# Performance work log

Measured on AMD Instinct MI355X. Metric: run time of the kernel, lower is better.

The kernel has to match this reference:

```python
import jax, jax.numpy as jnp
import numpy as np


def _phi(x):
    # ELU(x) + 1 feature map (positive kernel feature map)
    return jax.nn.elu(x) + 1.0


def setup_inputs() -> dict:
    key = jax.random.key(0)
    k1, k2, k3 = jax.random.split(key, 3)
    B, S, E = 4, 4096, 1024
    inputs = jax.random.normal(k1, (B, S, E), dtype=jnp.float32)
    mask = jnp.ones((B, S), dtype=jnp.float32)
    w_qkv = jax.random.normal(k2, (3 * E, E), dtype=jnp.float32) * (E ** -0.5)
    b_qkv = jax.random.normal(k3, (3 * E,), dtype=jnp.float32) * 0.02
    return {"inputs": inputs, "mask": mask, "w_qkv": w_qkv, "b_qkv": b_qkv, "num_heads": 16}


def reference(inputs, mask, w_qkv, b_qkv, num_heads):
    B, S, E = inputs.shape
    H = num_heads
    D = E // H
    # qkv projection: torch Linear is x @ W.T + b
    qkv = inputs @ w_qkv.T + b_qkv                     # (B, S, 3E)
    qkv = qkv.reshape(B, S, 3, H, D)
    q = qkv[:, :, 0]                                   # (B, S, H, D)
    k = qkv[:, :, 1]
    v = qkv[:, :, 2]
    # key masking (float multiply, as in einsum 'bshd,bs->bshd')
    k = k * mask[:, :, None, None]
    kq = _phi(q)                                       # (B, S, H, D)
    kk = _phi(k)                                       # (B, S, H, D)
    # kv outer-product accumulation over sequence: (B, H, M, D)
    kv = jnp.einsum('bshd,bshm->bhmd', kk, v)
    # normalizer
    z = 1.0 / (jnp.einsum('bshd,bhd->bsh', kq, kk.sum(axis=1)) + 1e-6)
    # final contraction
    attn = jnp.einsum('bshd,bhmd,bsh->bshm', kq, kv, z)  # (B, S, H, D)
    attn = attn.reshape(B, S, E)
    # NOTE: original forward computes a projection but returns `attn` (dropout is
    # identity at inference), so projection is dead code and omitted here.
    return attn
```

## Files before the change

### kernel.cpp

```cpp
#include <hip/hip_runtime.h>

typedef unsigned short u16;
typedef short bf16x8 __attribute__((ext_vector_type(8)));
typedef float f32x4 __attribute__((ext_vector_type(4)));
typedef u16 u16x8 __attribute__((ext_vector_type(8)));
typedef u16 u16x4 __attribute__((ext_vector_type(4)));

#define B_ 4
#define S_ 4096
#define E_ 1024
#define H_ 16
#define D_ 64
#define M_ 16384
#define N_ 3072
#define K_ 1024

__device__ __forceinline__ u16 f2b(float f) {
    unsigned x = __builtin_bit_cast(unsigned, f);
    return (u16)((x + 0x7fffu + ((x >> 16) & 1u)) >> 16);
}
__device__ __forceinline__ float b2f(u16 u) {
    unsigned x = ((unsigned)u) << 16;
    return __builtin_bit_cast(float, x);
}
__device__ __forceinline__ float phi_f(float x) { return x > 0.f ? x + 1.f : __expf(x); }

__device__ __forceinline__ void gload16(const void* g, void* l) {
    __builtin_amdgcn_global_load_lds((const __attribute__((address_space(1))) void*)g,
                                     (__attribute__((address_space(3))) void*)l, 16, 0, 0);
}

__global__ void cvt_bf16(const float* __restrict__ in, u16* __restrict__ out, int n8) {
    int stride = gridDim.x * blockDim.x;
    for (int i = blockIdx.x * blockDim.x + threadIdx.x; i < n8; i += stride) {
        const float4* p = (const float4*)(in + (size_t)i * 8);
        float4 a = p[0], b = p[1];
        u16x8 o;
        o[0] = f2b(a.x); o[1] = f2b(a.y); o[2] = f2b(a.z); o[3] = f2b(a.w);
        o[4] = f2b(b.x); o[5] = f2b(b.y); o[6] = f2b(b.z); o[7] = f2b(b.w);
        *(u16x8*)(out + (size_t)i * 8) = o;
    }
}


__device__ __forceinline__ void compute_tile(const char* ldsbase, int rowA, int rowB,
                                             int pc0, int pc1, f32x4 (&acc)[8][4])
{
    const char* bA = ldsbase + rowA;
    const char* bB = ldsbase + 32768 + rowB;
#pragma unroll
    for (int kk = 0; kk < 2; ++kk) {
        int pc = kk ? pc1 : pc0;
        bf16x8 a[8], bb[4];
#pragma unroll
        for (int mi = 0; mi < 8; ++mi) a[mi] = *(const bf16x8*)(bA + mi * 2048 + pc);
#pragma unroll
        for (int ni = 0; ni < 4; ++ni) bb[ni] = *(const bf16x8*)(bB + ni * 2048 + pc);
        __builtin_amdgcn_s_setprio(1);
#pragma unroll
        for (int mi = 0; mi < 8; ++mi)
#pragma unroll
            for (int ni = 0; ni < 4; ++ni)
                acc[mi][ni] = __builtin_amdgcn_mfma_f32_16x16x32_bf16(
                    a[mi], bb[ni], acc[mi][ni], 0, 0, 0);
        __builtin_amdgcn_s_setprio(0);
    }
}

__device__ __forceinline__ void stage_tile(const u16* gA, const u16* gB, char* ldsbase, int t)
{
#pragma unroll
    for (int i = 0; i < 4; ++i)
        gload16(gA + (size_t)i * 64 * K_, ldsbase + i * 8192 + t * 16);
#pragma unroll
    for (int i = 0; i < 4; ++i)
        gload16(gB + (size_t)i * 64 * K_, ldsbase + 32768 + i * 8192 + t * 16);
}

#define MEMFENCE asm volatile("" ::: "memory")

__global__ __launch_bounds__(512, 2) void gemm_qkv(
    const u16* __restrict__ Abf, const u16* __restrict__ Wbf,
    const float* __restrict__ bias, const float* __restrict__ mask,
    u16* __restrict__ KQ, u16* __restrict__ KKT, u16* __restrict__ VT)
{
    __shared__ __align__(16) char lds[131072];

    int wg  = blockIdx.x;
    int xcd = wg & 7, ii = wg >> 3;
    int tm  = xcd * 8 + ii / 12;
    int tn  = ii % 12;
    int m0 = tm << 8, n0 = tn << 8;

    int t = threadIdx.x;
    int l = t & 63, wid = t >> 6;
    int wr = wid >> 2, wc = wid & 3;
    int lg = l >> 4, lr = l & 15;

    int srow  = t >> 3;
    int scolE = ((t & 7) ^ (srow & 7)) << 3;
    const u16* gA = Abf + (size_t)(m0 + srow) * K_ + scolE;
    const u16* gB = Wbf + (size_t)(n0 + srow) * K_ + scolE;

    int rowA = (wr * 128 + lr) * 128;
    int rowB = (wc * 64 + lr) * 128;
    int pc0  = (lg * 16) ^ ((lr & 7) << 4);
    int pc1  = pc0 ^ 64;

    f32x4 acc[8][4] = {};

    stage_tile(gA, gB, lds, t);
    stage_tile(gA + 64, gB + 64, lds + 65536, t);
    asm volatile("s_waitcnt vmcnt(8)" ::: "memory");
    __builtin_amdgcn_s_barrier();
    MEMFENCE;

    for (int kt2 = 0; kt2 < 14; kt2 += 2) {
        compute_tile(lds, rowA, rowB, pc0, pc1, acc);
        MEMFENCE;
        __builtin_amdgcn_s_barrier();
        MEMFENCE;
        stage_tile(gA + (size_t)(kt2 + 2) * 64, gB + (size_t)(kt2 + 2) * 64, lds, t);
        asm volatile("s_waitcnt vmcnt(8)" ::: "memory");
        __builtin_amdgcn_s_barrier();
        MEMFENCE;
        compute_tile(lds + 65536, rowA, rowB, pc0, pc1, acc);
        MEMFENCE;
        __builtin_amdgcn_s_barrier();
        MEMFENCE;
        stage_tile(gA + (size_t)(kt2 + 3) * 64, gB + (size_t)(kt2 + 3) * 64, lds + 65536, t);
        asm volatile("s_waitcnt vmcnt(8)" ::: "memory");
        __builtin_amdgcn_s_barrier();
        MEMFENCE;
    }
    compute_tile(lds, rowA, rowB, pc0, pc1, acc);
    asm volatile("s_waitcnt vmcnt(0)" ::: "memory");
    __builtin_amdgcn_s_barrier();
    MEMFENCE;
    compute_tile(lds + 65536, rowA, rowB, pc0, pc1, acc);

    int part = n0 >> 10;

    float bv[4];
#pragma unroll
    for (int ni = 0; ni < 4; ++ni) bv[ni] = bias[n0 + wc * 64 + ni * 16 + lr];

    if (part == 0) {
#pragma unroll
        for (int mi = 0; mi < 8; ++mi)
#pragma unroll
            for (int j = 0; j < 4; ++j) {
                int row = m0 + wr * 128 + mi * 16 + lg * 4 + j;
#pragma unroll
                for (int ni = 0; ni < 4; ++ni) {
                    int col = n0 + wc * 64 + ni * 16 + lr;
                    KQ[(size_t)row * E_ + col] = f2b(phi_f(acc[mi][ni][j] + bv[ni]));
                }
            }
    } else {
        u16* dst0 = (part == 1) ? KKT : VT;
        int b  = m0 >> 12;
        int sl = m0 & (S_ - 1);
        int h  = ((tn & 3) << 2) | wc;
#pragma unroll
        for (int mi = 0; mi < 8; ++mi) {
            int sbase = sl + wr * 128 + mi * 16 + lg * 4;
            float mk[4];
#pragma unroll
            for (int j = 0; j < 4; ++j)
                mk[j] = (part == 1) ? mask[m0 + wr * 128 + mi * 16 + lg * 4 + j] : 1.f;
#pragma unroll
            for (int ni = 0; ni < 4; ++ni) {
                u16x4 o;
#pragma unroll
                for (int j = 0; j < 4; ++j) {
                    float v = acc[mi][ni][j] + bv[ni];
                    if (part == 1) v = phi_f(v * mk[j]);
                    o[j] = f2b(v);
                }
                int d = ni * 16 + lr;
                *(u16x4*)(dst0 + ((size_t)((b * H_ + h) * D_ + d)) * S_ + sbase) = o;
            }
        }
    }
}

__global__ __launch_bounds__(256) void kv_ksum_partial(
    const u16* __restrict__ VT, const u16* __restrict__ KKT,
    float* __restrict__ KVP, float* __restrict__ KSP)
{
    __shared__ __align__(16) u16 smem[8192];
    u16* As = smem;
    u16* Bs = smem + 4096;
    int bh = blockIdx.x;
    int ch = blockIdx.y;
    int s0 = ch << 8;
    int t = threadIdx.x;
    int l = t & 63, w = t >> 6;
    int lg = l >> 4, lr = l & 15;
    const u16* Ag = VT + (size_t)bh * (D_ * S_);
    const u16* Bg = KKT + (size_t)bh * (D_ * S_);
    int srow = t >> 3, scol = (t & 7) << 3;

    f32x4 acc[4] = {};
    float ks = 0.f;
    int kd = t >> 2;
    int kq4 = (t & 3) << 4;

    for (int kt = 0; kt < 4; ++kt) {
        __syncthreads();
        int sb = s0 + kt * 64;
#pragma unroll
        for (int i = 0; i < 2; ++i) {
            gload16(Ag + (size_t)(srow + i * 32) * S_ + sb + scol, As + i * 2048 + t * 8);
            gload16(Bg + (size_t)(srow + i * 32) * S_ + sb + scol, Bs + i * 2048 + t * 8);
        }
        __syncthreads();
#pragma unroll
        for (int i = 0; i < 16; ++i) ks += b2f(Bs[kd * 64 + kq4 + i]);
#pragma unroll
        for (int kh = 0; kh < 2; ++kh) {
            int ko = kh * 32 + lg * 8;
            bf16x8 a = *(const bf16x8*)&As[(w * 16 + lr) * 64 + ko];
#pragma unroll
            for (int ni = 0; ni < 4; ++ni) {
                bf16x8 bb = *(const bf16x8*)&Bs[(ni * 16 + lr) * 64 + ko];
                acc[ni] = __builtin_amdgcn_mfma_f32_16x16x32_bf16(a, bb, acc[ni], 0, 0, 0);
            }
        }
    }
    float* kvp = KVP + (size_t)ch * (64 * 4096) + bh * 4096;
#pragma unroll
    for (int ni = 0; ni < 4; ++ni)
#pragma unroll
        for (int j = 0; j < 4; ++j)
            kvp[(w * 16 + lg * 4 + j) * 64 + ni * 16 + lr] = acc[ni][j];
    ks += __shfl_xor(ks, 1);
    ks += __shfl_xor(ks, 2);
    if ((t & 3) == 0) KSP[ch * 4096 + bh * 64 + kd] = ks;
}

__global__ void reduce_kv(const float* __restrict__ KVP, const float* __restrict__ KSP,
                          float* __restrict__ KV, float* __restrict__ KSUM)
{
    int g = blockIdx.x * 256 + threadIdx.x;
#pragma unroll 1
    for (int i = g * 4; i < g * 4 + 4; ++i) {
        float s = 0.f;
#pragma unroll
        for (int c = 0; c < 16; ++c) s += KVP[(size_t)c * (64 * 4096) + i];
        KV[i] = s;
    }
    if (g < 4096) {
        float s = 0.f;
#pragma unroll
        for (int c = 0; c < 16; ++c) s += KSP[c * 4096 + g];
        KSUM[g] = s;
    }
}

__global__ __launch_bounds__(256) void attn_out(
    const u16* __restrict__ KQ, const float* __restrict__ KV,
    const float* __restrict__ KSUM, float* __restrict__ Out)
{
    __shared__ __align__(16) u16 kqs[16384];
    __shared__ __align__(16) u16 bsm[5120];
    __shared__ float den[256];
    int bh = blockIdx.x, ch = blockIdx.y;
    int b = bh >> 4, h = bh & 15;
    int t = threadIdx.x;
    int l = t & 63, w = t >> 6;
    int lg = l >> 4, lr = l & 15;
    size_t row0 = (size_t)b * S_ + ch * 256;
    int srow = t >> 3, scol = (t & 7) << 3;
#pragma unroll
    for (int i = 0; i < 8; ++i)
        gload16(KQ + (row0 + srow + i * 32) * E_ + h * 64 + scol, kqs + i * 2048 + t * 8);

    const float* kvg = KV + bh * 4096;
#pragma unroll
    for (int ii = 0; ii < 16; ii += 4) {
        float4 v = *(const float4*)(kvg + t * 16 + ii);
        u16x4 o; o[0] = f2b(v.x); o[1] = f2b(v.y); o[2] = f2b(v.z); o[3] = f2b(v.w);
        *(u16x4*)&bsm[t * 16 + ii] = o;
    }
    if (t < 64) bsm[4096 + t] = f2b(KSUM[bh * 64 + t]);
    for (int i = t; i < 960; i += 256) bsm[4160 + i] = 0;
    __syncthreads();

    f32x4 acc[4][5] = {};
#pragma unroll
    for (int kh = 0; kh < 2; ++kh) {
        int ko = kh * 32 + lg * 8;
        bf16x8 af[4];
#pragma unroll
        for (int mi = 0; mi < 4; ++mi)
            af[mi] = *(const bf16x8*)&kqs[(w * 64 + mi * 16 + lr) * 64 + ko];
#pragma unroll
        for (int ni = 0; ni < 5; ++ni) {
            bf16x8 bb = *(const bf16x8*)&bsm[(ni * 16 + lr) * 64 + ko];
#pragma unroll
            for (int mi = 0; mi < 4; ++mi)
                acc[mi][ni] = __builtin_amdgcn_mfma_f32_16x16x32_bf16(af[mi], bb, acc[mi][ni], 0, 0, 0);
        }
    }
    if (lr == 0) {
#pragma unroll
        for (int mi = 0; mi < 4; ++mi)
#pragma unroll
            for (int j = 0; j < 4; ++j)
                den[w * 64 + mi * 16 + lg * 4 + j] = acc[mi][4][j];
    }
    __syncthreads();
#pragma unroll
    for (int mi = 0; mi < 4; ++mi)
#pragma unroll
        for (int j = 0; j < 4; ++j) {
            int sl = w * 64 + mi * 16 + lg * 4 + j;
            float z = 1.f / (den[sl] + 1e-6f);
            float* op = Out + (row0 + sl) * E_ + h * 64;
#pragma unroll
            for (int ni = 0; ni < 4; ++ni)
                op[ni * 16 + lr] = acc[mi][ni][j] * z;
        }
}

extern "C" void kernel_launch(void* const* d_in, const int* in_sizes, int n_in,
                              void* d_out, int out_size, void* d_ws, size_t ws_size,
                              hipStream_t stream)
{
    const float* inputs = (const float*)d_in[0];
    const float* mask   = (const float*)d_in[1];
    const float* w_qkv  = (const float*)d_in[2];
    const float* b_qkv  = (const float*)d_in[3];

    u16* Abf = (u16*)d_ws;
    u16* Wbf = Abf + (size_t)M_ * K_;
    u16* KQ  = Wbf + (size_t)N_ * K_;
    float* KVP  = (float*)(KQ + (size_t)M_ * E_);
    float* KSP  = KVP + 16 * 64 * 4096;
    float* KV   = KSP + 16 * 4096;
    float* KSUM = KV + 64 * 4096;

    u16* KKT = (u16*)d_out;
    u16* VT  = KKT + (size_t)M_ * E_;

    cvt_bf16<<<2048, 256, 0, stream>>>(inputs, Abf, M_ * K_ / 8);
    cvt_bf16<<<768, 256, 0, stream>>>(w_qkv, Wbf, N_ * K_ / 8);
    gemm_qkv<<<768, 512, 0, stream>>>(Abf, Wbf, b_qkv, mask, KQ, KKT, VT);
    kv_ksum_partial<<<dim3(64, 16), 256, 0, stream>>>(VT, KKT, KVP, KSP);
    reduce_kv<<<256, 256, 0, stream>>>(KVP, KSP, KV, KSUM);
    attn_out<<<dim3(64, 16), 256, 0, stream>>>(KQ, KV, KSUM, (float*)d_out);
}
```

Before: 168.6 us.

## Interleave LDS reads, global-to-LDS staging and MFMA in fine-grained GEMM sub-stages

Restructures the QKV GEMM main loop into eight sub-stages per double-buffered tile pair. Each sub-stage reads a quarter of the A/B fragments from LDS, issues part of the next tile's global-to-LDS loads, and runs a 4x2 MFMA block, with barriers between them. A and B staging are split so B can be prefetched into the other buffer earlier. The aim is to overlap memory traffic with matrix math in a ping-pong schedule. In exchange it adds many more barriers and redundant clamped tail loads (tiles 15) that must stay correct with the vmcnt accounting.

```diff
diff --git a/kernel.cpp b/kernel.cpp
--- a/kernel.cpp
+++ b/kernel.cpp
@@ -29,6 +29,8 @@
     __builtin_amdgcn_global_load_lds((const __attribute__((address_space(1))) void*)g,
                                      (__attribute__((address_space(3))) void*)l, 16, 0, 0);
 }
+
+#define MEMFENCE asm volatile("" ::: "memory")
 
 __global__ void cvt_bf16(const float* __restrict__ in, u16* __restrict__ out, int n8) {
     int stride = gridDim.x * blockDim.x;
@@ -43,42 +45,6 @@
 }
 
 
-__device__ __forceinline__ void compute_tile(const char* ldsbase, int rowA, int rowB,
-                                             int pc0, int pc1, f32x4 (&acc)[8][4])
-{
-    const char* bA = ldsbase + rowA;
-    const char* bB = ldsbase + 32768 + rowB;
-#pragma unroll
-    for (int kk = 0; kk < 2; ++kk) {
-        int pc = kk ? pc1 : pc0;
-        bf16x8 a[8], bb[4];
-#pragma unroll
-        for (int mi = 0; mi < 8; ++mi) a[mi] = *(const bf16x8*)(bA + mi * 2048 + pc);
-#pragma unroll
-        for (int ni = 0; ni < 4; ++ni) bb[ni] = *(const bf16x8*)(bB + ni * 2048 + pc);
-        __builtin_amdgcn_s_setprio(1);
-#pragma unroll
-        for (int mi = 0; mi < 8; ++mi)
-#pragma unroll
-            for (int ni = 0; ni < 4; ++ni)
-                acc[mi][ni] = __builtin_amdgcn_mfma_f32_16x16x32_bf16(
-                    a[mi], bb[ni], acc[mi][ni], 0, 0, 0);
-        __builtin_amdgcn_s_setprio(0);
-    }
-}
-
-__device__ __forceinline__ void stage_tile(const u16* gA, const u16* gB, char* ldsbase, int t)
-{
-#pragma unroll
-    for (int i = 0; i < 4; ++i)
-        gload16(gA + (size_t)i * 64 * K_, ldsbase + i * 8192 + t * 16);
-#pragma unroll
-    for (int i = 0; i < 4; ++i)
-        gload16(gB + (size_t)i * 64 * K_, ldsbase + 32768 + i * 8192 + t * 16);
-}
-
-#define MEMFENCE asm volatile("" ::: "memory")
-
 __global__ __launch_bounds__(512, 2) void gemm_qkv(
     const u16* __restrict__ Abf, const u16* __restrict__ Wbf,
     const float* __restrict__ bias, const float* __restrict__ mask,
@@ -99,45 +65,68 @@
 
     int srow  = t >> 3;
     int scolE = ((t & 7) ^ (srow & 7)) << 3;
+    int t16   = t * 16;
+
     const u16* gA = Abf + (size_t)(m0 + srow) * K_ + scolE;
     const u16* gB = Wbf + (size_t)(n0 + srow) * K_ + scolE;
 
-    int rowA = (wr * 128 + lr) * 128;
-    int rowB = (wc * 64 + lr) * 128;
-    int pc0  = (lg * 16) ^ ((lr & 7) << 4);
-    int pc1  = pc0 ^ 64;
+    const char* aB = lds + (wr * 128 + lr) * 128;
+    const char* bB = lds + 32768 + (wc * 64 + lr) * 128;
+    int pc0 = (lg * 16) ^ ((lr & 7) << 4);
+    int pc1 = pc0 ^ 64;
 
     f32x4 acc[8][4] = {};
-
-    stage_tile(gA, gB, lds, t);
-    stage_tile(gA + 64, gB + 64, lds + 65536, t);
-    asm volatile("s_waitcnt vmcnt(8)" ::: "memory");
+    bf16x8 av[4][2], bv2[2][2];
+
+#define RD_A(BO, MI0) { _Pragma("unroll") for (int m_ = 0; m_ < 4; ++m_) { \
+    av[m_][0] = *(const bf16x8*)(aB + (BO) + (MI0 + m_) * 2048 + pc0); \
+    av[m_][1] = *(const bf16x8*)(aB + (BO) + (MI0 + m_) * 2048 + pc1); } }
+
+#define RD_B(BO, NI0) { _Pragma("unroll") for (int n_ = 0; n_ < 2; ++n_) { \
+    bv2[n_][0] = *(const bf16x8*)(bB + (BO) + (NI0 + n_) * 2048 + pc0); \
+    bv2[n_][1] = *(const bf16x8*)(bB + (BO) + (NI0 + n_) * 2048 + pc1); } }
+
+#define ST_A(TT, HI, BO) { \
+    gload16(gA + (size_t)((HI) * 64) * K_ + (TT) * 64, lds + (BO) + (HI) * 8192 + t16); \
+    gload16(gA + (size_t)((HI) * 64 + 128) * K_ + (TT) * 64, lds + (BO) + 16384 + (HI) * 8192 + t16); }
+
+#define ST_B(TT, PR, BO) { \
+    gload16(gB + (size_t)((PR) * 128) * K_ + (TT) * 64, lds + (BO) + 32768 + (PR) * 16384 + t16); \
+    gload16(gB + (size_t)((PR) * 128 + 64) * K_ + (TT) * 64, lds + (BO) + 32768 + (PR) * 16384 + 8192 + t16); }
+
+#define BAR { MEMFENCE; __builtin_amdgcn_s_barrier(); MEMFENCE; }
+
+#define MM(MI0, NI0) { __builtin_amdgcn_s_setprio(1); \
+    _Pragma("unroll") for (int m_ = 0; m_ < 4; ++m_) \
+    _Pragma("unroll") for (int n_ = 0; n_ < 2; ++n_) \
+    _Pragma("unroll") for (int h_ = 0; h_ < 2; ++h_) \
+        acc[(MI0) + m_][(NI0) + n_] = __builtin_amdgcn_mfma_f32_16x16x32_bf16( \
+            av[m_][h_], bv2[n_][h_], acc[(MI0) + m_][(NI0) + n_], 0, 0, 0); \
+    __builtin_amdgcn_s_setprio(0); }
+
+    ST_A(0, 0, 0); ST_A(0, 1, 0); ST_B(0, 0, 0); ST_B(0, 1, 0);
+    ST_A(1, 0, 65536); ST_A(1, 1, 65536);
+    asm volatile("s_waitcnt vmcnt(4)" ::: "memory");
     __builtin_amdgcn_s_barrier();
     MEMFENCE;
 
-    for (int kt2 = 0; kt2 < 14; kt2 += 2) {
-        compute_tile(lds, rowA, rowB, pc0, pc1, acc);
-        MEMFENCE;
-        __builtin_amdgcn_s_barrier();
-        MEMFENCE;
-        stage_tile(gA + (size_t)(kt2 + 2) * 64, gB + (size_t)(kt2 + 2) * 64, lds, t);
-        asm volatile("s_waitcnt vmcnt(8)" ::: "memory");
-        __builtin_amdgcn_s_barrier();
-        MEMFENCE;
-        compute_tile(lds + 65536, rowA, rowB, pc0, pc1, acc);
-        MEMFENCE;
-        __builtin_amdgcn_s_barrier();
-        MEMFENCE;
-        stage_tile(gA + (size_t)(kt2 + 3) * 64, gB + (size_t)(kt2 + 3) * 64, lds + 65536, t);
-        asm volatile("s_waitcnt vmcnt(8)" ::: "memory");
-        __builtin_amdgcn_s_barrier();
-        MEMFENCE;
-    }
-    compute_tile(lds, rowA, rowB, pc0, pc1, acc);
-    asm volatile("s_waitcnt vmcnt(0)" ::: "memory");
-    __builtin_amdgcn_s_barrier();
-    MEMFENCE;
-    compute_tile(lds + 65536, rowA, rowB, pc0, pc1, acc);
+#pragma unroll 1
+    for (int kt = 0; kt < 16; kt += 2) {
+        int tp2 = kt + 2 < 16 ? kt + 2 : 15;
+        int tp3 = kt + 3 < 16 ? kt + 3 : 15;
+        RD_A(0, 0); RD_B(0, 0); ST_B(kt + 1, 0, 65536); BAR; MM(0, 0); BAR;
+        RD_B(0, 2); ST_B(kt + 1, 1, 65536); BAR; MM(0, 2); BAR;
+        RD_A(0, 4); ST_A(tp2, 0, 0); BAR; MM(4, 2); BAR;
+        RD_B(0, 0); ST_A(tp2, 1, 0);
+        asm volatile("s_waitcnt vmcnt(4)" ::: "memory");
+        BAR; MM(4, 0); BAR;
+        RD_A(65536, 0); RD_B(65536, 0); ST_B(tp2, 0, 0); BAR; MM(0, 0); BAR;
+        RD_B(65536, 2); ST_B(tp2, 1, 0); BAR; MM(0, 2); BAR;
+        RD_A(65536, 4); ST_A(tp3, 0, 65536); BAR; MM(4, 2); BAR;
+        RD_B(65536, 0); ST_A(tp3, 1, 65536);
+        asm volatile("s_waitcnt vmcnt(4)" ::: "memory");
+        BAR; MM(4, 0); BAR;
+    }
 
     int part = n0 >> 10;
 
```

Measured after the change: 168.1 us. Within noise of the previous version (-0.3%).
